# Optimization experiments

Hardware: AMD Instinct MI355X
Metric: run time of the kernel (lower is better)

The kernel has to match this reference:

```python
import jax, jax.numpy as jnp
import numpy as np

DEPTH, BREADTH, N_HEADS = 6, 1024, 16
D_HEAD = BREADTH // N_HEADS
EPS = 1e-5


def layer_norm(x, g, b):
    m = jnp.mean(x, axis=-1, keepdims=True)
    v = jnp.mean(jnp.square(x - m), axis=-1, keepdims=True)
    return (x - m) * jax.lax.rsqrt(v + EPS) * g + b


def setup_inputs() -> dict:
    key = jax.random.key(0)
    ks = jax.random.split(key, 16)
    B, S, Dm, Dff = 4, 1024, BREADTH, 4 * BREADTH
    s = 0.02
    return {
        "x": jax.random.normal(ks[0], (B, S, Dm), dtype=jnp.float32),
        "mask": jnp.ones((B, S, S), dtype=jnp.int32),
        "wq": s * jax.random.normal(ks[1], (DEPTH, Dm, Dm), dtype=jnp.float32),
        "bq": jnp.zeros((DEPTH, Dm), dtype=jnp.float32),
        "wk": s * jax.random.normal(ks[2], (DEPTH, Dm, Dm), dtype=jnp.float32),
        "bk": jnp.zeros((DEPTH, Dm), dtype=jnp.float32),
        "wv": s * jax.random.normal(ks[3], (DEPTH, Dm, Dm), dtype=jnp.float32),
        "bv": jnp.zeros((DEPTH, Dm), dtype=jnp.float32),
        "wo": s * jax.random.normal(ks[4], (DEPTH, Dm, Dm), dtype=jnp.float32),
        "bo": jnp.zeros((DEPTH, Dm), dtype=jnp.float32),
        "w1": s * jax.random.normal(ks[5], (DEPTH, Dm, Dff), dtype=jnp.float32),
        "b1": jnp.zeros((DEPTH, Dff), dtype=jnp.float32),
        "w2": s * jax.random.normal(ks[6], (DEPTH, Dff, Dm), dtype=jnp.float32),
        "b2": jnp.zeros((DEPTH, Dm), dtype=jnp.float32),
        "ln1g": jnp.ones((DEPTH, Dm), dtype=jnp.float32),
        "ln1b": jnp.zeros((DEPTH, Dm), dtype=jnp.float32),
        "ln2g": jnp.ones((DEPTH, Dm), dtype=jnp.float32),
        "ln2b": jnp.zeros((DEPTH, Dm), dtype=jnp.float32),
        "lnfg": jnp.ones((Dm,), dtype=jnp.float32),
        "lnfb": jnp.zeros((Dm,), dtype=jnp.float32),
    }


def reference(x, mask, wq, bq, wk, bk, wv, bv, wo, bo, w1, b1, w2, b2,
              ln1g, ln1b, ln2g, ln2b, lnfg, lnfb):
    B, S, Dm = x.shape
    scale = 1.0 / jnp.sqrt(jnp.float32(D_HEAD))
    neg = jnp.float32(-1e9)
    mask_b = (mask == 0)[:, None]  # [B,1,S,S]

    def split_heads(t):  # [B,S,Dm] -> [B,H,S,d]
        return t.reshape(B, S, N_HEADS, D_HEAD).transpose(0, 2, 1, 3)

    for i in range(DEPTH):
        xn1 = layer_norm(x, ln1g[i], ln1b[i])  # attention branch input
        xn2 = layer_norm(x, ln2g[i], ln2b[i])  # FFN branch input (pre-attention, per original)

        q = split_heads(xn1 @ wq[i] + bq[i])
        k = split_heads(xn1 @ wk[i] + bk[i])
        v = split_heads(xn1 @ wv[i] + bv[i])
        scores = jnp.einsum("bhqd,bhkd->bhqk", q, k) * scale
        scores = jnp.where(mask_b, neg, scores)
        attn = jax.nn.softmax(scores, axis=-1)
        ctx = jnp.einsum("bhqk,bhkd->bhqd", attn, v)
        ctx = ctx.transpose(0, 2, 1, 3).reshape(B, S, Dm)
        x = x + (ctx @ wo[i] + bo[i])

        h = jax.nn.relu(xn2 @ w1[i] + b1[i])
        x = x + (h @ w2[i] + b2[i])

    return layer_norm(x, lnfg, lnfb)
```

## Files before the change

kernel.cpp:

```cpp
#include <hip/hip_runtime.h>
#include <hip/hip_bf16.h>
#include <stdint.h>

#define DEPTH 6
#define DM 1024
#define DFF 4096
#define NH 16
#define DH 64
#define BATCH 4
#define SEQ 1024
#define NTOK (BATCH*SEQ)
#define QKVLD 3072

using bf16x8 = __attribute__((ext_vector_type(8))) short;
using f32x4  = __attribute__((ext_vector_type(4))) float;
typedef unsigned short u16;

__device__ __forceinline__ u16 f2bf(float f) {
  union { float f; uint32_t u; } v; v.f = f;
  return (u16)((v.u + 0x7FFFu + ((v.u >> 16) & 1u)) >> 16);
}

__device__ __forceinline__ void async16(void* lds, const void* g) {
  __builtin_amdgcn_global_load_lds(
      (__attribute__((address_space(1))) void*)(unsigned long long)g,
      (__attribute__((address_space(3))) void*)(unsigned int)(unsigned long long)lds,
      16, 0, 0);
}

__global__ __launch_bounds__(256)
void prep(const float* __restrict__ wq, const float* __restrict__ wk,
          const float* __restrict__ wv, const float* __restrict__ wo,
          const float* __restrict__ w1, const float* __restrict__ w2,
          const float* __restrict__ bq, const float* __restrict__ bk,
          const float* __restrict__ bv,
          u16* __restrict__ wqkvT, u16* __restrict__ woT,
          u16* __restrict__ w1T, u16* __restrict__ w2T,
          float* __restrict__ bqkv) {
  const int bid = blockIdx.x;
  if (bid >= 12288) {
    const int t = (bid - 12288) * 256 + threadIdx.x;
    bqkv[t] = t < 1024 ? bq[t] : (t < 2048 ? bk[t - 1024] : bv[t - 2048]);
    return;
  }
  const float* w; u16* wt; int K, N, tile;
  if (bid < 3072)      { const int r = bid >> 10;
                         w = r == 0 ? wq : (r == 1 ? wk : wv);
                         wt = wqkvT + (size_t)r * 1024 * 1024; K = 1024; N = 1024; tile = bid & 1023; }
  else if (bid < 4096) { w = wo; wt = woT; K = 1024; N = 1024; tile = bid - 3072; }
  else if (bid < 8192) { w = w1; wt = w1T; K = 1024; N = 4096; tile = bid - 4096; }
  else                 { w = w2; wt = w2T; K = 4096; N = 1024; tile = bid - 8192; }
  const int ntn = N >> 5;
  const int k0 = (tile / ntn) << 5, n0 = (tile % ntn) << 5;

  __shared__ u16 t[32][33];
  const int tx = threadIdx.x & 31, ty = threadIdx.x >> 5;
  #pragma unroll
  for (int r = ty; r < 32; r += 8)
    t[r][tx] = f2bf(w[(size_t)(k0 + r) * N + n0 + tx]);
  __syncthreads();
  #pragma unroll
  for (int r = ty; r < 32; r += 8)
    wt[(size_t)(n0 + r) * K + k0 + tx] = t[tx][r];
}

__global__ __launch_bounds__(256)
void vtrans(const u16* __restrict__ qkv, u16* __restrict__ vt) {
  __shared__ u16 t[64][72];
  const int s0 = blockIdx.x * 64, c0 = blockIdx.y * 64, b = blockIdx.z;
  const int r = threadIdx.x >> 2, cq = threadIdx.x & 3;
  const u16* src = qkv + ((size_t)(b * SEQ + s0 + r)) * QKVLD + 2048 + c0 + cq * 16;
  *(bf16x8*)&t[r][cq * 16]     = *(const bf16x8*)(src);
  *(bf16x8*)&t[r][cq * 16 + 8] = *(const bf16x8*)(src + 8);
  __syncthreads();
  bf16x8 a, bvec;
  #pragma unroll
  for (int i = 0; i < 8; i++) a[i] = (short)t[cq * 16 + i][r];
  #pragma unroll
  for (int i = 0; i < 8; i++) bvec[i] = (short)t[cq * 16 + 8 + i][r];
  u16* dst = vt + ((size_t)(b * 1024 + c0 + r)) * SEQ + s0 + cq * 16;
  *(bf16x8*)dst = a;
  *(bf16x8*)(dst + 8) = bvec;
}

__global__ void flags_init(int* flags) {
  if (threadIdx.x < BATCH) flags[threadIdx.x] = 1;
}
__global__ void mask_flags(const int* __restrict__ mask, int* __restrict__ flags) {
  const size_t n = (size_t)BATCH * SEQ * SEQ;
  for (size_t i = (size_t)blockIdx.x * 256 + threadIdx.x; i < n; i += (size_t)gridDim.x * 256)
    if (mask[i] == 0) flags[i / ((size_t)SEQ * SEQ)] = 0;
}

__global__ __launch_bounds__(256)
void ln_dual(float* __restrict__ x, const float* __restrict__ slab,
             const float* __restrict__ g1, const float* __restrict__ b1v,
             const float* __restrict__ g2, const float* __restrict__ b2v,
             u16* __restrict__ o1, u16* __restrict__ o2) {
  const int row = blockIdx.x, tid = threadIdx.x;
  float4 v = ((const float4*)(x + (size_t)row * DM))[tid];
  if (slab) {
    const float4 sv = ((const float4*)(slab + (size_t)row * DM))[tid];
    v.x += sv.x; v.y += sv.y; v.z += sv.z; v.w += sv.w;
    ((float4*)(x + (size_t)row * DM))[tid] = v;
  }
  float s = v.x + v.y + v.z + v.w;
  float sq = v.x*v.x + v.y*v.y + v.z*v.z + v.w*v.w;
  #pragma unroll
  for (int o = 32; o; o >>= 1) { s += __shfl_xor(s, o); sq += __shfl_xor(sq, o); }
  __shared__ float red[8];
  const int lane = tid & 63, w = tid >> 6;
  if (lane == 0) { red[w] = s; red[4 + w] = sq; }
  __syncthreads();
  s = red[0] + red[1] + red[2] + red[3];
  sq = red[4] + red[5] + red[6] + red[7];
  const float mean = s * (1.0f / DM);
  const float rinv = rsqrtf(sq * (1.0f / DM) - mean * mean + 1e-5f);
  const float4 G1 = ((const float4*)g1)[tid], B1 = ((const float4*)b1v)[tid];
  const float4 G2 = ((const float4*)g2)[tid], B2 = ((const float4*)b2v)[tid];
  const float n0 = (v.x - mean) * rinv, n1 = (v.y - mean) * rinv;
  const float n2 = (v.z - mean) * rinv, n3 = (v.w - mean) * rinv;
  ushort4 a, bb;
  a.x = f2bf(n0*G1.x + B1.x); a.y = f2bf(n1*G1.y + B1.y);
  a.z = f2bf(n2*G1.z + B1.z); a.w = f2bf(n3*G1.w + B1.w);
  bb.x = f2bf(n0*G2.x + B2.x); bb.y = f2bf(n1*G2.y + B2.y);
  bb.z = f2bf(n2*G2.z + B2.z); bb.w = f2bf(n3*G2.w + B2.w);
  ((ushort4*)(o1 + (size_t)row * DM))[tid] = a;
  ((ushort4*)(o2 + (size_t)row * DM))[tid] = bb;
}

__global__ __launch_bounds__(256)
void ln_final(const float* __restrict__ x, const float* __restrict__ slab,
              const float* __restrict__ g, const float* __restrict__ b,
              float* __restrict__ out) {
  const int row = blockIdx.x, tid = threadIdx.x;
  float4 v = ((const float4*)(x + (size_t)row * DM))[tid];
  if (slab) {
    const float4 sv = ((const float4*)(slab + (size_t)row * DM))[tid];
    v.x += sv.x; v.y += sv.y; v.z += sv.z; v.w += sv.w;
  }
  float s = v.x + v.y + v.z + v.w;
  float sq = v.x*v.x + v.y*v.y + v.z*v.z + v.w*v.w;
  #pragma unroll
  for (int o = 32; o; o >>= 1) { s += __shfl_xor(s, o); sq += __shfl_xor(sq, o); }
  __shared__ float red[8];
  const int lane = tid & 63, w = tid >> 6;
  if (lane == 0) { red[w] = s; red[4 + w] = sq; }
  __syncthreads();
  s = red[0] + red[1] + red[2] + red[3];
  sq = red[4] + red[5] + red[6] + red[7];
  const float mean = s * (1.0f / DM);
  const float rinv = rsqrtf(sq * (1.0f / DM) - mean * mean + 1e-5f);
  const float4 G = ((const float4*)g)[tid], B = ((const float4*)b)[tid];
  float4 o;
  o.x = (v.x - mean) * rinv * G.x + B.x;
  o.y = (v.y - mean) * rinv * G.y + B.y;
  o.z = (v.z - mean) * rinv * G.z + B.z;
  o.w = (v.w - mean) * rinv * G.w + B.w;
  ((float4*)(out + (size_t)row * DM))[tid] = o;
}

template<int EPI, int BN, int SPLITK>
__global__ __launch_bounds__(256)
void gemm_bt(const u16* __restrict__ A, const u16* __restrict__ BT,
             const float* __restrict__ bias,
             u16* __restrict__ Cb, float* __restrict__ Cf, float* __restrict__ Cf2,
             int M, int N, int K) {
  constexpr int WCn = BN / 64;
  constexpr int WR  = 4 / WCn;
  constexpr int MF  = 8 / WR;
  constexpr int WRS = 128 / WR;
  constexpr int ASZ = 128 * 32;
  constexpr int BSZ = BN * 32;
  __shared__ u16 As[2 * ASZ];
  __shared__ u16 Bs[2 * BSZ];
  const int tid = threadIdx.x;
  const int lane = tid & 63, wave = tid >> 6;
  const int wr = wave / WCn, wc = wave % WCn;
  const int l16 = lane & 15, lhi = lane >> 4;

  const int ntn = N / BN;
  const int ntiles = (M >> 7) * ntn;
  const int nwg = ntiles * SPLITK;
  int wg = (int)blockIdx.x;
  if ((nwg & 7) == 0) { const int q = nwg >> 3; wg = (wg & 7) * q + (wg >> 3); }
  const int tile = wg / SPLITK, ks = wg % SPLITK;
  const int tm = tile / ntn, tn = tile % ntn;
  const int KL = K / SPLITK;

  const int srow = tid >> 2, sc = (tid & 3) * 8;
  const u16* Ag0 = A  + (size_t)(tm * 128 + srow) * K + ks * KL + sc;
  const u16* Bg0 = BT + (size_t)(tn * BN + srow) * K + ks * KL + sc;
  const size_t rstep = (size_t)64 * K;

  auto stage = [&](int buf, int k0) {
    async16(As + buf * ASZ + tid * 8, Ag0 + k0);
    async16(As + buf * ASZ + 2048 + tid * 8, Ag0 + rstep + k0);
    async16(Bs + buf * BSZ + tid * 8, Bg0 + k0);
    if constexpr (BN == 128) async16(Bs + buf * BSZ + 2048 + tid * 8, Bg0 + rstep + k0);
  };

  f32x4 acc[MF][4];
  #pragma unroll
  for (int m = 0; m < MF; m++)
    #pragma unroll
    for (int n = 0; n < 4; n++)
      #pragma unroll
      for (int j = 0; j < 4; j++) acc[m][n][j] = 0.0f;

  stage(0, 0);
  __syncthreads();
  int cur = 0;
  for (int k0 = 0; k0 < KL; k0 += 32) {
    if (k0 + 32 < KL) stage(cur ^ 1, k0 + 32);
    const u16* Ab = As + cur * ASZ;
    const u16* Bb = Bs + cur * BSZ;
    bf16x8 af[MF], bfv[4];
    #pragma unroll
    for (int m = 0; m < MF; m++)
      af[m] = *(const bf16x8*)&Ab[(wr * WRS + m * 16 + l16) * 32 + lhi * 8];
    #pragma unroll
    for (int n = 0; n < 4; n++)
      bfv[n] = *(const bf16x8*)&Bb[(wc * 64 + n * 16 + l16) * 32 + lhi * 8];
    #pragma unroll
    for (int m = 0; m < MF; m++)
      #pragma unroll
      for (int n = 0; n < 4; n++)
        acc[m][n] = __builtin_amdgcn_mfma_f32_16x16x32_bf16(af[m], bfv[n], acc[m][n], 0, 0, 0);
    __syncthreads();
    cur ^= 1;
  }

  const int row0 = tm * 128 + wr * WRS + lhi * 4;
  const int col0 = tn * BN + wc * 64 + l16;
  #pragma unroll
  for (int n = 0; n < 4; n++) {
    const int col = col0 + n * 16;
    const float bv = bias[col];
    #pragma unroll
    for (int m = 0; m < MF; m++) {
      #pragma unroll
      for (int j = 0; j < 4; j++) {
        const int row = row0 + m * 16 + j;
        const size_t idx = (size_t)row * N + col;
        float v = acc[m][n][j];
        if constexpr (EPI == 3) {
          if (ks == 0) Cf[idx] += v + bv;
          else         Cf2[idx] += v;
        } else if constexpr (EPI == 5) {
          if (ks == 0) Cf[idx] += v + bv;
          else         Cf2[idx] = v;
        } else {
          v += bv;
          if constexpr (EPI == 1) v = fmaxf(v, 0.0f);
          if constexpr (EPI <= 1) Cb[idx] = f2bf(v);
          else                    Cf[idx] += v;
        }
      }
    }
  }
}

__global__ __launch_bounds__(256, 4)
void attn(const u16* __restrict__ QKV, const u16* __restrict__ VTg,
          u16* __restrict__ Octx,
          const int* __restrict__ mask, const int* __restrict__ flags) {
  __shared__ u16 Ks[2 * 64 * 64];
  __shared__ u16 VTs[2 * 64 * 64];
  __shared__ u16 Ps[4 * 16 * 64];
  const int tid = threadIdx.x, lane = tid & 63, wv = tid >> 6;
  const int l16 = lane & 15, lhi = lane >> 4;
  const int bid = blockIdx.x;
  const int pair = bid >> 4, qblk = bid & 15;
  const int b = pair >> 4, h = pair & 15;
  const int hoff = h * DH;
  const int q0 = qblk * 64 + wv * 16;
  const size_t tokbase = (size_t)b * SEQ;
  const size_t vbase = ((size_t)b * 1024 + hoff) * SEQ;

  bf16x8 qf[2];
  #pragma unroll
  for (int ds = 0; ds < 2; ds++)
    qf[ds] = *(const bf16x8*)&QKV[(tokbase + q0 + l16) * QKVLD + hoff + ds * 32 + lhi * 8];

  f32x4 oacc[4];
  #pragma unroll
  for (int nt = 0; nt < 4; nt++)
    #pragma unroll
    for (int j = 0; j < 4; j++) oacc[nt][j] = 0.0f;
  float mrun = -1e30f, lrun = 0.0f;

  const int allone = flags[b];
  char* PwB = (char*)(Ps + wv * (16 * 64));
  const int xw = (l16 & 7) << 4;

  const int srow0 = tid >> 3, scb0 = (tid & 7) ^ (srow0 & 7);
  const int srow1 = (tid + 256) >> 3, scb1 = (tid & 7) ^ (srow1 & 7);
  const int shfl_src = (lane & 48) + ((lane >> 4) << 2);

  auto stage = [&](int buf, int kt) {
    async16((char*)Ks + buf * 8192 + tid * 16,
            &QKV[(tokbase + kt + srow0) * QKVLD + 1024 + hoff + scb0 * 8]);
    async16((char*)Ks + buf * 8192 + 4096 + tid * 16,
            &QKV[(tokbase + kt + srow1) * QKVLD + 1024 + hoff + scb1 * 8]);
    async16((char*)VTs + buf * 8192 + tid * 16,
            &VTg[vbase + (size_t)srow0 * SEQ + kt + scb0 * 8]);
    async16((char*)VTs + buf * 8192 + 4096 + tid * 16,
            &VTg[vbase + (size_t)srow1 * SEQ + kt + scb1 * 8]);
  };

  stage(0, 0);
  __syncthreads();
  int cur = 0;
  for (int kt = 0; kt < SEQ; kt += 64) {
    if (kt + 64 < SEQ) stage(cur ^ 1, kt + 64);
    char* KsB = (char*)Ks + cur * 8192;
    char* VTB = (char*)VTs + cur * 8192;

    f32x4 sacc[4];
    #pragma unroll
    for (int nt = 0; nt < 4; nt++)
      #pragma unroll
      for (int j = 0; j < 4; j++) sacc[nt][j] = 0.0f;
    #pragma unroll
    for (int ds = 0; ds < 2; ds++) {
      bf16x8 kf[4];
      #pragma unroll
      for (int nt = 0; nt < 4; nt++) {
        const int rk = nt * 16 + l16;
        kf[nt] = *(const bf16x8*)(KsB + ((rk * 128 + ds * 64 + lhi * 16) ^ ((rk & 7) << 4)));
      }
      #pragma unroll
      for (int nt = 0; nt < 4; nt++)
        sacc[nt] = __builtin_amdgcn_mfma_f32_16x16x32_bf16(kf[nt], qf[ds], sacc[nt], 0, 0, 0);
    }
    #pragma unroll
    for (int nt = 0; nt < 4; nt++)
      #pragma unroll
      for (int j = 0; j < 4; j++) sacc[nt][j] *= 0.125f;

    if (!allone) {
      const int qg = q0 + l16;
      #pragma unroll
      for (int nt = 0; nt < 4; nt++)
        #pragma unroll
        for (int j = 0; j < 4; j++) {
          const int kc = kt + nt * 16 + lhi * 4 + j;
          if (mask[(tokbase + qg) * SEQ + kc] == 0) sacc[nt][j] = -1e9f;
        }
    }

    float tmax = -1e30f;
    #pragma unroll
    for (int nt = 0; nt < 4; nt++)
      #pragma unroll
      for (int j = 0; j < 4; j++) tmax = fmaxf(tmax, sacc[nt][j]);
    tmax = fmaxf(tmax, __shfl_xor(tmax, 16));
    tmax = fmaxf(tmax, __shfl_xor(tmax, 32));
    const float mnew = fmaxf(mrun, tmax);
    const float corr = __expf(mrun - mnew);
    float p[4][4];
    float tsum = 0.0f;
    #pragma unroll
    for (int nt = 0; nt < 4; nt++)
      #pragma unroll
      for (int j = 0; j < 4; j++) { p[nt][j] = __expf(sacc[nt][j] - mnew); tsum += p[nt][j]; }
    tsum += __shfl_xor(tsum, 16);
    tsum += __shfl_xor(tsum, 32);
    lrun = lrun * corr + tsum;
    mrun = mnew;

    #pragma unroll
    for (int nt = 0; nt < 4; nt++) {
      const uint32_t lo = (uint32_t)f2bf(p[nt][0]) | ((uint32_t)f2bf(p[nt][1]) << 16);
      const uint32_t hi = (uint32_t)f2bf(p[nt][2]) | ((uint32_t)f2bf(p[nt][3]) << 16);
      *(uint64_t*)(PwB + ((l16 * 128 + nt * 32 + lhi * 8) ^ xw)) =
          (uint64_t)lo | ((uint64_t)hi << 32);
    }

    float cj[4];
    #pragma unroll
    for (int j = 0; j < 4; j++) cj[j] = __shfl(corr, shfl_src + j);
    #pragma unroll
    for (int nt = 0; nt < 4; nt++)
      #pragma unroll
      for (int j = 0; j < 4; j++) oacc[nt][j] *= cj[j];

    #pragma unroll
    for (int ksl = 0; ksl < 2; ksl++) {
      const bf16x8 pf = *(const bf16x8*)(PwB + ((l16 * 128 + ksl * 64 + lhi * 16) ^ xw));
      #pragma unroll
      for (int nt = 0; nt < 4; nt++) {
        const int dr = nt * 16 + l16;
        const bf16x8 vf = *(const bf16x8*)(VTB + ((dr * 128 + ksl * 64 + lhi * 16) ^ ((dr & 7) << 4)));
        oacc[nt] = __builtin_amdgcn_mfma_f32_16x16x32_bf16(pf, vf, oacc[nt], 0, 0, 0);
      }
    }
    __syncthreads();
    cur ^= 1;
  }

  const float linv = 1.0f / lrun;
  float lj[4];
  #pragma unroll
  for (int j = 0; j < 4; j++) lj[j] = __shfl(linv, shfl_src + j);
  #pragma unroll
  for (int j = 0; j < 4; j++) {
    const size_t rowg = (tokbase + q0 + lhi * 4 + j) * DM + hoff;
    #pragma unroll
    for (int nt = 0; nt < 4; nt++)
      Octx[rowg + nt * 16 + l16] = f2bf(oacc[nt][j] * lj[j]);
  }
}

extern "C" void kernel_launch(void* const* d_in, const int* in_sizes, int n_in,
                              void* d_out, int out_size, void* d_ws, size_t ws_size,
                              hipStream_t stream) {
  const float* x    = (const float*)d_in[0];
  const int*   mask = (const int*)d_in[1];
  const float* wq = (const float*)d_in[2];
  const float* bq = (const float*)d_in[3];
  const float* wk = (const float*)d_in[4];
  const float* bk = (const float*)d_in[5];
  const float* wvp = (const float*)d_in[6];
  const float* bv = (const float*)d_in[7];
  const float* wo = (const float*)d_in[8];
  const float* bo = (const float*)d_in[9];
  const float* w1 = (const float*)d_in[10];
  const float* b1 = (const float*)d_in[11];
  const float* w2 = (const float*)d_in[12];
  const float* b2 = (const float*)d_in[13];
  const float* ln1g = (const float*)d_in[14];
  const float* ln1b = (const float*)d_in[15];
  const float* ln2g = (const float*)d_in[16];
  const float* ln2b = (const float*)d_in[17];
  const float* lnfg = (const float*)d_in[18];
  const float* lnfb = (const float*)d_in[19];

  char* ws = (char*)d_ws;
  float* xbuf = (float*)(ws);
  u16* xn1  = (u16*)(ws + ((size_t)16 << 20));
  u16* xn2  = (u16*)(ws + ((size_t)24 << 20));
  u16* qkv  = (u16*)(ws + ((size_t)32 << 20));
  u16* ctx  = (u16*)(ws + ((size_t)56 << 20));
  u16* hb   = (u16*)(ws + ((size_t)32 << 20));
  u16* wqkvT= (u16*)(ws + ((size_t)64 << 20));
  u16* woT  = (u16*)(ws + ((size_t)70 << 20));
  u16* w1T  = (u16*)(ws + ((size_t)72 << 20));
  u16* w2T  = (u16*)(ws + ((size_t)80 << 20));
  u16* vT   = (u16*)(ws + ((size_t)88 << 20));
  float* bqkv = (float*)(ws + ((size_t)96 << 20));
  int* flags  = (int*)(ws + ((size_t)96 << 20) + 65536);
  float* slab = (float*)(ws + ((size_t)97 << 20));

  const bool split = ws_size >= ((size_t)113 << 20);

  hipMemcpyAsync(xbuf, x, (size_t)NTOK * DM * sizeof(float),
                 hipMemcpyDeviceToDevice, stream);
  flags_init<<<1, 64, 0, stream>>>(flags);
  mask_flags<<<1024, 256, 0, stream>>>(mask, flags);

  auto wgs128 = [](int M, int N) { return dim3((unsigned)((M >> 7) * (N >> 7))); };
  auto wgs64  = [](int M, int N) { return dim3((unsigned)((M >> 7) * (N >> 6))); };

  for (int i = 0; i < DEPTH; i++) {
    prep<<<12300, 256, 0, stream>>>(
        wq  + (size_t)i * DM * DM,  wk + (size_t)i * DM * DM,
        wvp + (size_t)i * DM * DM,  wo + (size_t)i * DM * DM,
        w1  + (size_t)i * DM * DFF, w2 + (size_t)i * DFF * DM,
        bq + i * DM, bk + i * DM, bv + i * DM,
        wqkvT, woT, w1T, w2T, bqkv);

    ln_dual<<<NTOK, 256, 0, stream>>>(xbuf, (split && i > 0) ? slab : nullptr,
                                      ln1g + i * DM, ln1b + i * DM,
                                      ln2g + i * DM, ln2b + i * DM, xn1, xn2);

    gemm_bt<0, 128, 1><<<wgs128(NTOK, QKVLD), 256, 0, stream>>>(
        xn1, wqkvT, bqkv, qkv, nullptr, nullptr, NTOK, QKVLD, DM);
    vtrans<<<dim3(16, 16, 4), 256, 0, stream>>>(qkv, vT);

    attn<<<1024, 256, 0, stream>>>(qkv, vT, ctx, mask, flags);

    if (split) {
      gemm_bt<5, 64, 2><<<dim3((NTOK >> 7) * (DM >> 6) * 2), 256, 0, stream>>>(
          ctx, woT, bo + i * DM, nullptr, xbuf, slab, NTOK, DM, DM);
    } else {
      gemm_bt<2, 64, 1><<<wgs64(NTOK, DM), 256, 0, stream>>>(
          ctx, woT, bo + i * DM, nullptr, xbuf, nullptr, NTOK, DM, DM);
    }

    gemm_bt<1, 128, 1><<<wgs128(NTOK, DFF), 256, 0, stream>>>(
        xn2, w1T, b1 + i * DFF, hb, nullptr, nullptr, NTOK, DFF, DM);

    if (split) {
      gemm_bt<3, 64, 2><<<dim3((NTOK >> 7) * (DM >> 6) * 2), 256, 0, stream>>>(
          hb, w2T, b2 + i * DM, nullptr, xbuf, slab, NTOK, DM, DFF);
    } else {
      gemm_bt<2, 64, 1><<<wgs64(NTOK, DM), 256, 0, stream>>>(
          hb, w2T, b2 + i * DM, nullptr, xbuf, nullptr, NTOK, DM, DFF);
    }
  }

  ln_final<<<NTOK, 256, 0, stream>>>(xbuf, split ? slab : nullptr,
                                     lnfg, lnfb, (float*)d_out);
}
```

Before: 1.527 ms.

## Switch GEMM to 256x64 tiles with eight waves per block

Replaces the templated 128xBN GEMM tile with a fixed 256x64 tile using 512 threads, where each of eight waves computes a 32x64 strip. The intent is more waves per block to hide latency and a uniform tile shape for all projections. It lowers MFMA work per wave per k-step and changes the A/B reuse balance, which may hurt the wide-N GEMMs.

Result: slower. 1.567 ms (+2.6%).

```diff
diff --git a/kernel.cpp b/kernel.cpp
--- a/kernel.cpp
+++ b/kernel.cpp
@@ -160,27 +160,20 @@
   ((float4*)(out + (size_t)row * DM))[tid] = o;
 }
 
-template<int EPI, int BN, int SPLITK>
-__global__ __launch_bounds__(256)
+template<int EPI, int SPLITK>
+__global__ __launch_bounds__(512)
 void gemm_bt(const u16* __restrict__ A, const u16* __restrict__ BT,
              const float* __restrict__ bias,
              u16* __restrict__ Cb, float* __restrict__ Cf, float* __restrict__ Cf2,
              int M, int N, int K) {
-  constexpr int WCn = BN / 64;
-  constexpr int WR  = 4 / WCn;
-  constexpr int MF  = 8 / WR;
-  constexpr int WRS = 128 / WR;
-  constexpr int ASZ = 128 * 32;
-  constexpr int BSZ = BN * 32;
-  __shared__ u16 As[2 * ASZ];
-  __shared__ u16 Bs[2 * BSZ];
+  __shared__ u16 As[2 * 256 * 32];
+  __shared__ u16 Bs[2 * 64 * 32];
   const int tid = threadIdx.x;
   const int lane = tid & 63, wave = tid >> 6;
-  const int wr = wave / WCn, wc = wave % WCn;
   const int l16 = lane & 15, lhi = lane >> 4;
 
-  const int ntn = N / BN;
-  const int ntiles = (M >> 7) * ntn;
+  const int ntn = N >> 6;
+  const int ntiles = (M >> 8) * ntn;
   const int nwg = ntiles * SPLITK;
   int wg = (int)blockIdx.x;
   if ((nwg & 7) == 0) { const int q = nwg >> 3; wg = (wg & 7) * q + (wg >> 3); }
@@ -189,20 +182,19 @@
   const int KL = K / SPLITK;
 
   const int srow = tid >> 2, sc = (tid & 3) * 8;
-  const u16* Ag0 = A  + (size_t)(tm * 128 + srow) * K + ks * KL + sc;
-  const u16* Bg0 = BT + (size_t)(tn * BN + srow) * K + ks * KL + sc;
-  const size_t rstep = (size_t)64 * K;
+  const u16* Ag0 = A  + (size_t)(tm * 256 + srow) * K + ks * KL + sc;
+  const u16* Bg0 = BT + (size_t)(tn * 64 + srow) * K + ks * KL + sc;
+  const size_t rstep = (size_t)128 * K;
 
   auto stage = [&](int buf, int k0) {
-    async16(As + buf * ASZ + tid * 8, Ag0 + k0);
-    async16(As + buf * ASZ + 2048 + tid * 8, Ag0 + rstep + k0);
-    async16(Bs + buf * BSZ + tid * 8, Bg0 + k0);
-    if constexpr (BN == 128) async16(Bs + buf * BSZ + 2048 + tid * 8, Bg0 + rstep + k0);
+    async16(As + buf * 8192 + tid * 8, Ag0 + k0);
+    async16(As + buf * 8192 + 4096 + tid * 8, Ag0 + rstep + k0);
+    if (tid < 256) async16(Bs + buf * 2048 + tid * 8, Bg0 + k0);
   };
 
-  f32x4 acc[MF][4];
-  #pragma unroll
-  for (int m = 0; m < MF; m++)
+  f32x4 acc[2][4];
+  #pragma unroll
+  for (int m = 0; m < 2; m++)
     #pragma unroll
     for (int n = 0; n < 4; n++)
       #pragma unroll
@@ -213,17 +205,17 @@
   int cur = 0;
   for (int k0 = 0; k0 < KL; k0 += 32) {
     if (k0 + 32 < KL) stage(cur ^ 1, k0 + 32);
-    const u16* Ab = As + cur * ASZ;
-    const u16* Bb = Bs + cur * BSZ;
-    bf16x8 af[MF], bfv[4];
-    #pragma unroll
-    for (int m = 0; m < MF; m++)
-      af[m] = *(const bf16x8*)&Ab[(wr * WRS + m * 16 + l16) * 32 + lhi * 8];
+    const u16* Ab = As + cur * 8192;
+    const u16* Bb = Bs + cur * 2048;
+    bf16x8 af[2], bfv[4];
+    #pragma unroll
+    for (int m = 0; m < 2; m++)
+      af[m] = *(const bf16x8*)&Ab[(wave * 32 + m * 16 + l16) * 32 + lhi * 8];
     #pragma unroll
     for (int n = 0; n < 4; n++)
-      bfv[n] = *(const bf16x8*)&Bb[(wc * 64 + n * 16 + l16) * 32 + lhi * 8];
-    #pragma unroll
-    for (int m = 0; m < MF; m++)
+      bfv[n] = *(const bf16x8*)&Bb[(n * 16 + l16) * 32 + lhi * 8];
+    #pragma unroll
+    for (int m = 0; m < 2; m++)
       #pragma unroll
       for (int n = 0; n < 4; n++)
         acc[m][n] = __builtin_amdgcn_mfma_f32_16x16x32_bf16(af[m], bfv[n], acc[m][n], 0, 0, 0);
@@ -231,14 +223,14 @@
     cur ^= 1;
   }
 
-  const int row0 = tm * 128 + wr * WRS + lhi * 4;
-  const int col0 = tn * BN + wc * 64 + l16;
+  const int row0 = tm * 256 + wave * 32 + lhi * 4;
+  const int col0 = tn * 64 + l16;
   #pragma unroll
   for (int n = 0; n < 4; n++) {
     const int col = col0 + n * 16;
     const float bv = bias[col];
     #pragma unroll
-    for (int m = 0; m < MF; m++) {
+    for (int m = 0; m < 2; m++) {
       #pragma unroll
       for (int j = 0; j < 4; j++) {
         const int row = row0 + m * 16 + j;
@@ -460,8 +452,9 @@
   flags_init<<<1, 64, 0, stream>>>(flags);
   mask_flags<<<1024, 256, 0, stream>>>(mask, flags);
 
-  auto wgs128 = [](int M, int N) { return dim3((unsigned)((M >> 7) * (N >> 7))); };
-  auto wgs64  = [](int M, int N) { return dim3((unsigned)((M >> 7) * (N >> 6))); };
+  auto wgs = [](int M, int N, int S) {
+    return dim3((unsigned)((M >> 8) * (N >> 6) * S));
+  };
 
   for (int i = 0; i < DEPTH; i++) {
     prep<<<12300, 256, 0, stream>>>(
@@ -475,28 +468,28 @@
                                       ln1g + i * DM, ln1b + i * DM,
                                       ln2g + i * DM, ln2b + i * DM, xn1, xn2);
 
-    gemm_bt<0, 128, 1><<<wgs128(NTOK, QKVLD), 256, 0, stream>>>(
+    gemm_bt<0, 1><<<wgs(NTOK, QKVLD, 1), 512, 0, stream>>>(
         xn1, wqkvT, bqkv, qkv, nullptr, nullptr, NTOK, QKVLD, DM);
     vtrans<<<dim3(16, 16, 4), 256, 0, stream>>>(qkv, vT);
 
     attn<<<1024, 256, 0, stream>>>(qkv, vT, ctx, mask, flags);
 
     if (split) {
-      gemm_bt<5, 64, 2><<<dim3((NTOK >> 7) * (DM >> 6) * 2), 256, 0, stream>>>(
+      gemm_bt<5, 2><<<wgs(NTOK, DM, 2), 512, 0, stream>>>(
           ctx, woT, bo + i * DM, nullptr, xbuf, slab, NTOK, DM, DM);
     } else {
-      gemm_bt<2, 64, 1><<<wgs64(NTOK, DM), 256, 0, stream>>>(
+      gemm_bt<2, 1><<<wgs(NTOK, DM, 1), 512, 0, stream>>>(
           ctx, woT, bo + i * DM, nullptr, xbuf, nullptr, NTOK, DM, DM);
     }
 
-    gemm_bt<1, 128, 1><<<wgs128(NTOK, DFF), 256, 0, stream>>>(
+    gemm_bt<1, 1><<<wgs(NTOK, DFF, 1), 512, 0, stream>>>(
         xn2, w1T, b1 + i * DFF, hb, nullptr, nullptr, NTOK, DFF, DM);
 
     if (split) {
-      gemm_bt<3, 64, 2><<<dim3((NTOK >> 7) * (DM >> 6) * 2), 256, 0, stream>>>(
+      gemm_bt<3, 2><<<wgs(NTOK, DM, 2), 512, 0, stream>>>(
           hb, w2T, b2 + i * DM, nullptr, xbuf, slab, NTOK, DM, DFF);
     } else {
-      gemm_bt<2, 64, 1><<<wgs64(NTOK, DM), 256, 0, stream>>>(
+      gemm_bt<2, 1><<<wgs(NTOK, DM, 1), 512, 0, stream>>>(
           hb, w2T, b2 + i * DM, nullptr, xbuf, nullptr, NTOK, DM, DFF);
     }
   }
```

## Triple-buffer GEMM LDS staging with explicit vmcnt gating

Applied to the files above, without the earlier changes.

Replaces the double-buffered async global-to-LDS staging in the bf16 GEMM with a three-deep ring buffer. Loads run up to three K-steps ahead, and each iteration waits only for its own tile via hand-written s_waitcnt vmcnt counts instead of a full __syncthreads drain. The aim is to hide global memory latency behind MFMA work. In exchange it uses 1.5x the LDS, which may reduce occupancy, and the hard-coded vmcnt values must match the exact number of loads issued per stage.

Result: slower. 1.587 ms (+3.9%).

```diff
diff --git a/kernel.cpp b/kernel.cpp
--- a/kernel.cpp
+++ b/kernel.cpp
@@ -27,6 +27,8 @@
       (__attribute__((address_space(3))) void*)(unsigned int)(unsigned long long)lds,
       16, 0, 0);
 }
+
+#define BARRIER() do { __builtin_amdgcn_s_barrier(); asm volatile("" ::: "memory"); } while (0)
 
 __global__ __launch_bounds__(256)
 void prep(const float* __restrict__ wq, const float* __restrict__ wk,
@@ -172,8 +174,8 @@
   constexpr int WRS = 128 / WR;
   constexpr int ASZ = 128 * 32;
   constexpr int BSZ = BN * 32;
-  __shared__ u16 As[2 * ASZ];
-  __shared__ u16 Bs[2 * BSZ];
+  __shared__ u16 As[3 * ASZ];
+  __shared__ u16 Bs[3 * BSZ];
   const int tid = threadIdx.x;
   const int lane = tid & 63, wave = tid >> 6;
   const int wr = wave / WCn, wc = wave % WCn;
@@ -187,18 +189,31 @@
   const int tile = wg / SPLITK, ks = wg % SPLITK;
   const int tm = tile / ntn, tn = tile % ntn;
   const int KL = K / SPLITK;
+  const int NT = KL >> 5;
 
   const int srow = tid >> 2, sc = (tid & 3) * 8;
   const u16* Ag0 = A  + (size_t)(tm * 128 + srow) * K + ks * KL + sc;
   const u16* Bg0 = BT + (size_t)(tn * BN + srow) * K + ks * KL + sc;
   const size_t rstep = (size_t)64 * K;
 
-  auto stage = [&](int buf, int k0) {
-    async16(As + buf * ASZ + tid * 8, Ag0 + k0);
-    async16(As + buf * ASZ + 2048 + tid * 8, Ag0 + rstep + k0);
-    async16(Bs + buf * BSZ + tid * 8, Bg0 + k0);
-    if constexpr (BN == 128) async16(Bs + buf * BSZ + 2048 + tid * 8, Bg0 + rstep + k0);
+  auto stage = [&](int buf, int t) {
+    async16(As + buf * ASZ + tid * 8, Ag0 + t * 32);
+    async16(As + buf * ASZ + 2048 + tid * 8, Ag0 + rstep + t * 32);
+    async16(Bs + buf * BSZ + tid * 8, Bg0 + t * 32);
+    if constexpr (BN == 128) async16(Bs + buf * BSZ + 2048 + tid * 8, Bg0 + rstep + t * 32);
   };
+  auto gate = [&](int t) {
+    const int rem = NT - 1 - t;
+    if constexpr (BN == 128) {
+      if (rem >= 2)      asm volatile("s_waitcnt vmcnt(8)" ::: "memory");
+      else if (rem == 1) asm volatile("s_waitcnt vmcnt(4)" ::: "memory");
+      else               asm volatile("s_waitcnt vmcnt(0)" ::: "memory");
+    } else {
+      if (rem >= 2)      asm volatile("s_waitcnt vmcnt(6)" ::: "memory");
+      else if (rem == 1) asm volatile("s_waitcnt vmcnt(3)" ::: "memory");
+      else               asm volatile("s_waitcnt vmcnt(0)" ::: "memory");
+    }
+  };
 
   f32x4 acc[MF][4];
   #pragma unroll
@@ -208,13 +223,14 @@
       #pragma unroll
       for (int j = 0; j < 4; j++) acc[m][n][j] = 0.0f;
 
-  stage(0, 0);
-  __syncthreads();
-  int cur = 0;
-  for (int k0 = 0; k0 < KL; k0 += 32) {
-    if (k0 + 32 < KL) stage(cur ^ 1, k0 + 32);
-    const u16* Ab = As + cur * ASZ;
-    const u16* Bb = Bs + cur * BSZ;
+  stage(0, 0); stage(1, 1); stage(2, 2);
+
+  int buf = 0;
+  for (int t = 0; t < NT; ++t) {
+    gate(t);
+    BARRIER();
+    const u16* Ab = As + buf * ASZ;
+    const u16* Bb = Bs + buf * BSZ;
     bf16x8 af[MF], bfv[4];
     #pragma unroll
     for (int m = 0; m < MF; m++)
@@ -227,8 +243,9 @@
       #pragma unroll
       for (int n = 0; n < 4; n++)
         acc[m][n] = __builtin_amdgcn_mfma_f32_16x16x32_bf16(af[m], bfv[n], acc[m][n], 0, 0, 0);
-    __syncthreads();
-    cur ^= 1;
+    BARRIER();
+    if (t + 3 < NT) stage(buf, t + 3);
+    buf = buf == 2 ? 0 : buf + 1;
   }
 
   const int row0 = tm * 128 + wr * WRS + lhi * 4;
```
